# Kernel tuning notes

Hardware: AMD Instinct MI355X
Metric: run time of the kernel (lower is better)

## Reference

```python
import jax, jax.numpy as jnp
import numpy as np

N_NODES = 100000
N_EDGES = 3200000
IN_F = 128
HID = 32


def setup_inputs() -> dict:
    key = jax.random.key(0)
    k = jax.random.split(key, 8)
    x = jax.random.normal(k[0], (N_NODES, IN_F), dtype=jnp.float32)
    edge_index = jax.random.randint(k[1], (2, N_EDGES), 0, N_NODES, dtype=jnp.int64)
    edge_weight = jax.random.uniform(k[2], (N_EDGES,), dtype=jnp.float32)
    # GCN conv weight (in -> 32) and bias, then Linear(32 -> 1)
    s1 = 1.0 / np.sqrt(IN_F)
    s2 = 1.0 / np.sqrt(HID)
    W1 = jax.random.uniform(k[3], (IN_F, HID), dtype=jnp.float32, minval=-s1, maxval=s1)
    b1 = jax.random.uniform(k[4], (HID,), dtype=jnp.float32, minval=-s1, maxval=s1)
    W2 = jax.random.uniform(k[5], (HID, 1), dtype=jnp.float32, minval=-s2, maxval=s2)
    b2 = jax.random.uniform(k[6], (1,), dtype=jnp.float32, minval=-s2, maxval=s2)
    return {"x": x, "edge_index": edge_index, "edge_weight": edge_weight,
            "W1": W1, "b1": b1, "W2": W2, "b2": b2}


def gcn_conv(x, edge_index, edge_weight, W, b):
    N = x.shape[0]
    src = edge_index[0]
    dst = edge_index[1]
    loop = jnp.arange(N, dtype=edge_index.dtype)
    row = jnp.concatenate([dst, loop])  # aggregation targets
    col = jnp.concatenate([src, loop])  # message sources
    w = jnp.concatenate([edge_weight, jnp.ones((N,), dtype=x.dtype)])
    deg = jax.ops.segment_sum(w, row, num_segments=N)
    dinv = jnp.where(deg > 0, deg ** -0.5, 0.0).astype(x.dtype)
    norm = dinv[row] * w * dinv[col]  # [E+N]
    h = x @ W  # [N, 32]  transform before gather (cheaper)
    msgs = norm[:, None] * h[col]  # [E+N, 32]
    agg = jax.ops.segment_sum(msgs, row, num_segments=N)  # [N, 32]
    return agg + b


def reference(x, edge_index, edge_weight, W1, b1, W2, b2):
    h = gcn_conv(x, edge_index, edge_weight, W1, b1)
    h = jax.nn.relu(h)
    return h @ W2 + b2  # [N, 1]
```

## Files before the change

kernel.cpp:

```cpp
#include <hip/hip_runtime.h>
#include <hip/hip_bf16.h>
#include <hip/hip_fp16.h>

#define NN 100000
#define NE 3200000
#define IN_F 128
#define HID 32

#define BNODES 196
#define NB 511
#define NBP1 (NB + 1)
#define PBLK 768
#define EPB 4168
#define SSPAN 6912

typedef __hip_bfloat16 bf16;
typedef __attribute__((ext_vector_type(8))) short s16x8;
typedef __attribute__((ext_vector_type(4))) float f32x4;

__global__ __launch_bounds__(512) void k_part(const int* __restrict__ ei,
                                              const float* __restrict__ ew,
                                              int* __restrict__ offs,
                                              uint2* __restrict__ raw) {
    __shared__ int hist[NB];
    __shared__ int start[NB];
    __shared__ int wtot8[8];
    __shared__ __align__(16) uint2 sp[EPB];

    int t = threadIdx.x;
    int blk = blockIdx.x;
    if (t < NB) hist[t] = 0;
    __syncthreads();

    unsigned pk[10]; unsigned wb[10]; int bkt[10];
    int base_e = blk * EPB;
#pragma unroll
    for (int j = 0; j < 5; j++) {
        int p = j * 512 + t;
        int e = base_e + 2 * p;
        bool v = (p < (EPB / 2)) && (e < NE);
        if (v) {
            int2   s2 = *(const int2*)(ei + e);
            int2   d2 = *(const int2*)(ei + NE + e);
            float2 w2 = *(const float2*)(ew + e);
            int bk0 = d2.x / BNODES;
            bkt[2 * j]     = bk0;
            pk[2 * j]      = (unsigned)s2.x | ((unsigned)(d2.x - bk0 * BNODES) << 20);
            wb[2 * j]      = __float_as_uint(w2.x);
            int bk1 = d2.y / BNODES;
            bkt[2 * j + 1] = bk1;
            pk[2 * j + 1]  = (unsigned)s2.y | ((unsigned)(d2.y - bk1 * BNODES) << 20);
            wb[2 * j + 1]  = __float_as_uint(w2.y);
        } else { bkt[2 * j] = -1; bkt[2 * j + 1] = -1; }
    }
#pragma unroll
    for (int j = 0; j < 10; j++)
        if (bkt[j] >= 0) atomicAdd(&hist[bkt[j]], 1);
    __syncthreads();

    int h = (t < NB) ? hist[t] : 0;
    int lane = t & 63;
    int incl = h;
#pragma unroll
    for (int off = 1; off < 64; off <<= 1) {
        int up = __shfl_up(incl, off, 64);
        if (lane >= off) incl += up;
    }
    int wid = t >> 6;
    if (lane == 63) wtot8[wid] = incl;
    __syncthreads();
    int woff = 0;
    for (int wj = 0; wj < wid; wj++) woff += wtot8[wj];
    int exc = woff + incl - h;
    if (t < NB) start[t] = exc;
    __syncthreads();

    int total = start[NB - 1] + hist[NB - 1];
    int* orow = offs + (size_t)blk * NBP1;
    if (t < NB) orow[t] = start[t];
    if (t == 0) orow[NB] = total;
    __syncthreads();

#pragma unroll
    for (int j = 0; j < 10; j++) {
        if (bkt[j] >= 0) {
            int pos = atomicAdd(&start[bkt[j]], 1);
            sp[pos] = make_uint2(pk[j], wb[j]);
        }
    }
    __syncthreads();

    uint2* r = raw + (size_t)blk * EPB;
    int tot2 = total >> 1;
    const uint4* sp4 = (const uint4*)sp;
    uint4* r4 = (uint4*)r;
    for (int i = t; i < tot2; i += 512) r4[i] = sp4[i];
    if (t == 0 && (total & 1)) r[total - 1] = sp[total - 1];
}

__global__ __launch_bounds__(256) void k_trans(const int* __restrict__ in, int* __restrict__ out) {
    __shared__ int tile[32][33];
    int c0 = blockIdx.x * 32, r0 = blockIdx.y * 32;
    int tx = threadIdx.x & 31, ty = threadIdx.x >> 5;
    for (int i = ty; i < 32; i += 8) {
        int r = r0 + i, c = c0 + tx;
        if (r < PBLK && c < NBP1) tile[i][tx] = in[(size_t)r * NBP1 + c];
    }
    __syncthreads();
    for (int i = ty; i < 32; i += 8) {
        int c = c0 + i, r = r0 + tx;
        if (c < NBP1 && r < PBLK) out[(size_t)c * PBLK + r] = tile[tx][i];
    }
}

__global__ __launch_bounds__(512) void k_deg(const int* __restrict__ offsT,
                                             const uint2* __restrict__ raw,
                                             float* __restrict__ dinv) {
    __shared__ unsigned short runid[SSPAN];
    __shared__ int P[PBLK + 1];
    __shared__ int basearr[PBLK];
    __shared__ float wsum[BNODES];
    __shared__ int wt8[8];

    int t = threadIdx.x;
    int b = blockIdx.x;
    if (t < BNODES) wsum[t] = 0.f;

    int e0 = 2 * t, e1 = 2 * t + 1;
    int l0 = 0, l1 = 0, o0v = 0, o1v = 0;
    if (e0 < PBLK) {
        o0v = offsT[(size_t)b * PBLK + e0];
        l0  = offsT[(size_t)(b + 1) * PBLK + e0] - o0v;
    }
    if (e1 < PBLK) {
        o1v = offsT[(size_t)b * PBLK + e1];
        l1  = offsT[(size_t)(b + 1) * PBLK + e1] - o1v;
    }
    int psum = l0 + l1;
    int lane = t & 63;
    int incl = psum;
#pragma unroll
    for (int off = 1; off < 64; off <<= 1) {
        int up = __shfl_up(incl, off, 64);
        if (lane >= off) incl += up;
    }
    int wid = t >> 6;
    if (lane == 63) wt8[wid] = incl;
    __syncthreads();
    int woff = 0;
    for (int wj = 0; wj < wid; wj++) woff += wt8[wj];
    int exc = woff + incl - psum;
    if (e0 < PBLK) { P[e0] = exc;      basearr[e0] = o0v - exc; }
    if (e1 < PBLK) { P[e1] = exc + l0; basearr[e1] = o1v - (exc + l0); }
    if (t == 0) {
        int s = 0;
#pragma unroll
        for (int j = 0; j < 8; j++) s += wt8[j];
        P[PBLK] = s;
    }
    __syncthreads();

    int total = min(P[PBLK], SSPAN);

    for (int r = t; r < PBLK; r += 512) {
        int p0 = P[r], p1 = min(P[r + 1], SSPAN);
        for (int i = p0; i < p1; i++) runid[i] = (unsigned short)r;
    }
    __syncthreads();

#pragma unroll
    for (int k = 0; k < 14; k++) {
        int d = t + k * 512;
        if (d < total) {
            int r = runid[d];
            uint2 rec = raw[(size_t)r * EPB + (basearr[r] + d)];
            atomicAdd(&wsum[(rec.x >> 20) & 255], __uint_as_float(rec.y));
        }
    }
    __syncthreads();

    if (t < BNODES) {
        int node = b * BNODES + t;
        if (node < NN) dinv[node] = rsqrtf(wsum[t] + 1.0f);
    }
}

__global__ void k_w1frag(const float* __restrict__ W1, unsigned short* __restrict__ wfrag) {
    int lane = threadIdx.x;
    int q = lane >> 4;
    int n0 = lane & 15;
#pragma unroll
    for (int ks = 0; ks < 4; ks++) {
#pragma unroll
        for (int nt = 0; nt < 2; nt++) {
            int fi = ks * 2 + nt;
            int n = n0 + 16 * nt;
#pragma unroll
            for (int j = 0; j < 8; j++) {
                int k = ks * 32 + q * 8 + j;
                float v = W1[k * HID + n];
                __hip_bfloat16 bv = __float2bfloat16(v);
                wfrag[((size_t)fi * 64 + lane) * 8 + j] = *(unsigned short*)&bv;
            }
        }
    }
}

__global__ __launch_bounds__(256) void k_hs(const float* __restrict__ x,
                                            const unsigned short* __restrict__ wfrag,
                                            const float* __restrict__ dinv,
                                            bf16* __restrict__ hs) {
    int t = threadIdx.x;
    int lane = t & 63;
    int wv = t >> 6;
    int base = blockIdx.x * 64 + wv * 16;
    int m = lane & 15;
    int q = lane >> 4;
    int node = base + m;

    s16x8 wf[8];
    const s16x8* wp = (const s16x8*)wfrag;
#pragma unroll
    for (int fi = 0; fi < 8; fi++) wf[fi] = wp[fi * 64 + lane];

    f32x4 acc0 = {0.f, 0.f, 0.f, 0.f};
    f32x4 acc1 = {0.f, 0.f, 0.f, 0.f};

    const float* rowp = x + (size_t)node * IN_F + q * 8;
    bool valid = (node < NN);

#pragma unroll
    for (int ks = 0; ks < 4; ks++) {
        float4 f0 = {0,0,0,0}, f1 = {0,0,0,0};
        if (valid) {
            const float4* xr = (const float4*)(rowp + ks * 32);
            f0 = xr[0]; f1 = xr[1];
        }
        union { s16x8 v; unsigned u32[4]; } af;
        __hip_bfloat162 p0 = __float22bfloat162_rn({f0.x, f0.y});
        __hip_bfloat162 p1 = __float22bfloat162_rn({f0.z, f0.w});
        __hip_bfloat162 p2 = __float22bfloat162_rn({f1.x, f1.y});
        __hip_bfloat162 p3 = __float22bfloat162_rn({f1.z, f1.w});
        af.u32[0] = *(unsigned*)&p0;
        af.u32[1] = *(unsigned*)&p1;
        af.u32[2] = *(unsigned*)&p2;
        af.u32[3] = *(unsigned*)&p3;
        acc0 = __builtin_amdgcn_mfma_f32_16x16x32_bf16(af.v, wf[ks * 2 + 0], acc0, 0, 0, 0);
        acc1 = __builtin_amdgcn_mfma_f32_16x16x32_bf16(af.v, wf[ks * 2 + 1], acc1, 0, 0, 0);
    }

    int f = lane & 15;
#pragma unroll
    for (int r = 0; r < 4; r++) {
        int n2 = base + q * 4 + r;
        if (n2 < NN) {
            float dv = dinv[n2];
            hs[(size_t)n2 * HID + f]      = __float2bfloat16(dv * acc0[r]);
            hs[(size_t)n2 * HID + f + 16] = __float2bfloat16(dv * acc1[r]);
        }
    }
}

__global__ __launch_bounds__(512) void k_agg(const int* __restrict__ offsT,
                                             const uint2* __restrict__ raw,
                                             const bf16* __restrict__ hs,
                                             const float* __restrict__ dinv,
                                             const float* __restrict__ b1, const float* __restrict__ W2,
                                             const float* __restrict__ b2, float* __restrict__ out) {
    __shared__ uint2 se[SSPAN];
    __shared__ int P[PBLK + 1];
    __shared__ int basearr[PBLK];
    __shared__ int hist[BNODES];
    __shared__ int scanbuf[BNODES];
    __shared__ int cur[BNODES];
    __shared__ int wt8[8];

    unsigned short* runid = (unsigned short*)se;

    int t = threadIdx.x;
    int b = blockIdx.x;
    if (t < BNODES) hist[t] = 0;

    int e0 = 2 * t, e1 = 2 * t + 1;
    int l0 = 0, l1 = 0, o0v = 0, o1v = 0;
    if (e0 < PBLK) {
        o0v = offsT[(size_t)b * PBLK + e0];
        l0  = offsT[(size_t)(b + 1) * PBLK + e0] - o0v;
    }
    if (e1 < PBLK) {
        o1v = offsT[(size_t)b * PBLK + e1];
        l1  = offsT[(size_t)(b + 1) * PBLK + e1] - o1v;
    }
    int psum = l0 + l1;
    int lane = t & 63;
    int incl = psum;
#pragma unroll
    for (int off = 1; off < 64; off <<= 1) {
        int up = __shfl_up(incl, off, 64);
        if (lane >= off) incl += up;
    }
    int wid = t >> 6;
    if (lane == 63) wt8[wid] = incl;
    __syncthreads();
    int woff = 0;
    for (int wj = 0; wj < wid; wj++) woff += wt8[wj];
    int exc = woff + incl - psum;
    if (e0 < PBLK) { P[e0] = exc;      basearr[e0] = o0v - exc; }
    if (e1 < PBLK) { P[e1] = exc + l0; basearr[e1] = o1v - (exc + l0); }
    if (t == 0) {
        int s = 0;
#pragma unroll
        for (int j = 0; j < 8; j++) s += wt8[j];
        P[PBLK] = s;
    }
    __syncthreads();

    int total = min(P[PBLK], SSPAN);

    for (int r = t; r < PBLK; r += 512) {
        int p0 = P[r], p1 = min(P[r + 1], SSPAN);
        for (int i = p0; i < p1; i++) runid[i] = (unsigned short)r;
    }
    __syncthreads();

    uint2 rr[14];
#pragma unroll
    for (int k = 0; k < 14; k++) {
        int d = t + k * 512;
        if (d < total) {
            int r = runid[d];
            uint2 rec = raw[(size_t)r * EPB + (basearr[r] + d)];
            rr[k] = rec;
            int dl = (rec.x >> 20) & 255;
            atomicAdd(&hist[dl], 1);
        }
    }
    __syncthreads();

    if (t < BNODES) scanbuf[t] = hist[t];
    __syncthreads();
    for (int off = 1; off < BNODES; off <<= 1) {
        int v = 0;
        if (t < BNODES && t >= off) v = scanbuf[t - off];
        __syncthreads();
        if (t < BNODES) scanbuf[t] += v;
        __syncthreads();
    }
    if (t < BNODES) cur[t] = scanbuf[t] - hist[t];
    __syncthreads();

#pragma unroll
    for (int k = 0; k < 14; k++) {
        int d = t + k * 512;
        if (d < total) {
            uint2 rec = rr[k];
            int dl = (rec.x >> 20) & 255;
            int pos = atomicAdd(&cur[dl], 1);
            se[pos] = make_uint2(rec.x & 0xFFFFF, rec.y);
        }
    }
    __syncthreads();

    int gid = t >> 4;
    int l = t & 15;
    const __hip_bfloat162* hs2 = (const __hip_bfloat162*)hs;
    for (int dl = gid; dl < BNODES; dl += 32) {
        int cnt = hist[dl];
        int rs = scanbuf[dl] - cnt;
        float a0 = 0.f, a1 = 0.f;
        int full = cnt & ~7;
        int bse = 0;
        for (; bse < full; bse += 8) {
            uint2 q0 = se[rs + bse + 0];
            uint2 q1 = se[rs + bse + 1];
            uint2 q2 = se[rs + bse + 2];
            uint2 q3 = se[rs + bse + 3];
            uint2 q4 = se[rs + bse + 4];
            uint2 q5 = se[rs + bse + 5];
            uint2 q6 = se[rs + bse + 6];
            uint2 q7 = se[rs + bse + 7];
            __hip_bfloat162 h0 = hs2[(size_t)q0.x * 16 + l];
            __hip_bfloat162 h1 = hs2[(size_t)q1.x * 16 + l];
            __hip_bfloat162 h2 = hs2[(size_t)q2.x * 16 + l];
            __hip_bfloat162 h3 = hs2[(size_t)q3.x * 16 + l];
            __hip_bfloat162 h4 = hs2[(size_t)q4.x * 16 + l];
            __hip_bfloat162 h5 = hs2[(size_t)q5.x * 16 + l];
            __hip_bfloat162 h6 = hs2[(size_t)q6.x * 16 + l];
            __hip_bfloat162 h7 = hs2[(size_t)q7.x * 16 + l];
            float2 f0 = __bfloat1622float2(h0); a0 += __uint_as_float(q0.y) * f0.x; a1 += __uint_as_float(q0.y) * f0.y;
            float2 f1 = __bfloat1622float2(h1); a0 += __uint_as_float(q1.y) * f1.x; a1 += __uint_as_float(q1.y) * f1.y;
            float2 f2 = __bfloat1622float2(h2); a0 += __uint_as_float(q2.y) * f2.x; a1 += __uint_as_float(q2.y) * f2.y;
            float2 f3 = __bfloat1622float2(h3); a0 += __uint_as_float(q3.y) * f3.x; a1 += __uint_as_float(q3.y) * f3.y;
            float2 f4 = __bfloat1622float2(h4); a0 += __uint_as_float(q4.y) * f4.x; a1 += __uint_as_float(q4.y) * f4.y;
            float2 f5 = __bfloat1622float2(h5); a0 += __uint_as_float(q5.y) * f5.x; a1 += __uint_as_float(q5.y) * f5.y;
            float2 f6 = __bfloat1622float2(h6); a0 += __uint_as_float(q6.y) * f6.x; a1 += __uint_as_float(q6.y) * f6.y;
            float2 f7 = __bfloat1622float2(h7); a0 += __uint_as_float(q7.y) * f7.x; a1 += __uint_as_float(q7.y) * f7.y;
        }
        if (bse < cnt) {
            int rem = cnt - bse;
            uint2 q0 = se[rs + bse];
            uint2 q1 = se[rs + bse + (rem > 1 ? 1 : 0)];
            uint2 q2 = se[rs + bse + (rem > 2 ? 2 : 0)];
            uint2 q3 = se[rs + bse + (rem > 3 ? 3 : 0)];
            uint2 q4 = se[rs + bse + (rem > 4 ? 4 : 0)];
            uint2 q5 = se[rs + bse + (rem > 5 ? 5 : 0)];
            uint2 q6 = se[rs + bse + (rem > 6 ? 6 : 0)];
            float w0 = __uint_as_float(q0.y);
            float w1 = rem > 1 ? __uint_as_float(q1.y) : 0.f;
            float w2 = rem > 2 ? __uint_as_float(q2.y) : 0.f;
            float w3 = rem > 3 ? __uint_as_float(q3.y) : 0.f;
            float w4 = rem > 4 ? __uint_as_float(q4.y) : 0.f;
            float w5 = rem > 5 ? __uint_as_float(q5.y) : 0.f;
            float w6 = rem > 6 ? __uint_as_float(q6.y) : 0.f;
            __hip_bfloat162 h0 = hs2[(size_t)q0.x * 16 + l];
            __hip_bfloat162 h1 = hs2[(size_t)q1.x * 16 + l];
            __hip_bfloat162 h2 = hs2[(size_t)q2.x * 16 + l];
            __hip_bfloat162 h3 = hs2[(size_t)q3.x * 16 + l];
            __hip_bfloat162 h4 = hs2[(size_t)q4.x * 16 + l];
            __hip_bfloat162 h5 = hs2[(size_t)q5.x * 16 + l];
            __hip_bfloat162 h6 = hs2[(size_t)q6.x * 16 + l];
            float2 f0 = __bfloat1622float2(h0); a0 += w0 * f0.x; a1 += w0 * f0.y;
            float2 f1 = __bfloat1622float2(h1); a0 += w1 * f1.x; a1 += w1 * f1.y;
            float2 f2 = __bfloat1622float2(h2); a0 += w2 * f2.x; a1 += w2 * f2.y;
            float2 f3 = __bfloat1622float2(h3); a0 += w3 * f3.x; a1 += w3 * f3.y;
            float2 f4 = __bfloat1622float2(h4); a0 += w4 * f4.x; a1 += w4 * f4.y;
            float2 f5 = __bfloat1622float2(h5); a0 += w5 * f5.x; a1 += w5 * f5.y;
            float2 f6 = __bfloat1622float2(h6); a0 += w6 * f6.x; a1 += w6 * f6.y;
        }
        int node = b * BNODES + dl;
        if (node < NN) {
            float dv = dinv[node];
            float2 fs = __bfloat1622float2(hs2[(size_t)node * 16 + l]);
            float v0 = dv * (a0 + fs.x) + b1[2 * l];
            float v1 = dv * (a1 + fs.y) + b1[2 * l + 1];
            v0 = fmaxf(v0, 0.f);
            v1 = fmaxf(v1, 0.f);
            float ps = v0 * W2[2 * l] + v1 * W2[2 * l + 1];
#pragma unroll
            for (int m2 = 8; m2 >= 1; m2 >>= 1) ps += __shfl_xor(ps, m2, 16);
            if (l == 0) out[node] = ps + b2[0];
        }
    }
}

extern "C" void kernel_launch(void* const* d_in, const int* in_sizes, int n_in,
                              void* d_out, int out_size, void* d_ws, size_t ws_size,
                              hipStream_t stream) {
    const float* x  = (const float*)d_in[0];
    const int*   ei = (const int*)d_in[1];
    const float* ew = (const float*)d_in[2];
    const float* W1 = (const float*)d_in[3];
    const float* b1 = (const float*)d_in[4];
    const float* W2 = (const float*)d_in[5];
    const float* b2 = (const float*)d_in[6];
    float* out = (float*)d_out;

    char* ws = (char*)d_ws;
    uint2*          raw      = (uint2*)         (ws + 0);
    int*            offs     = (int*)           (ws + 25608192);
    int*            offsT    = (int*)           (ws + 27181056);
    bf16*           hs       = (bf16*)          (ws + 28753920);
    float*          dinv     = (float*)         (ws + 35153920);
    unsigned short* wfrag    = (unsigned short*)(ws + 35553920);

    k_w1frag<<<1, 64, 0, stream>>>(W1, wfrag);
    k_part<<<PBLK, 512, 0, stream>>>(ei, ew, offs, raw);
    k_trans<<<dim3((NBP1 + 31) / 32, (PBLK + 31) / 32), 256, 0, stream>>>(offs, offsT);
    k_deg<<<NB, 512, 0, stream>>>(offsT, raw, dinv);
    k_hs<<<(NN + 63) / 64, 256, 0, stream>>>(x, wfrag, dinv, hs);
    k_agg<<<NB, 512, 0, stream>>>(offsT, raw, hs, dinv, b1, W2, b2, out);
}
```

Baseline: 204.5 us.

## Halve node buckets per block and drop the offsets transpose kernel

Destination buckets shrink from 196 to 98 nodes, so the degree and aggregation kernels launch twice as many blocks, each with half the shared-memory span. The partition kernel's scan now handles two buckets per thread. The separate transpose kernel is removed, and the consumers read the per-partition offset table directly with strided column accesses. This saves one launch and one pass over the offsets table, in exchange for uncoalesced offset reads and a tighter per-bucket edge capacity that random degree variation has to fit within.

```diff
diff --git a/kernel.cpp b/kernel.cpp
--- a/kernel.cpp
+++ b/kernel.cpp
@@ -7,12 +7,12 @@
 #define IN_F 128
 #define HID 32
 
-#define BNODES 196
-#define NB 511
+#define BNODES 98
+#define NB 1021
 #define NBP1 (NB + 1)
 #define PBLK 768
 #define EPB 4168
-#define SSPAN 6912
+#define SSPAN 3584
 
 typedef __hip_bfloat16 bf16;
 typedef __attribute__((ext_vector_type(8))) short s16x8;
@@ -29,7 +29,7 @@
 
     int t = threadIdx.x;
     int blk = blockIdx.x;
-    if (t < NB) hist[t] = 0;
+    for (int b = t; b < NB; b += 512) hist[b] = 0;
     __syncthreads();
 
     unsigned pk[10]; unsigned wb[10]; int bkt[10];
@@ -58,9 +58,12 @@
         if (bkt[j] >= 0) atomicAdd(&hist[bkt[j]], 1);
     __syncthreads();
 
-    int h = (t < NB) ? hist[t] : 0;
+    int e0 = 2 * t, e1 = 2 * t + 1;
+    int h0 = (e0 < NB) ? hist[e0] : 0;
+    int h1 = (e1 < NB) ? hist[e1] : 0;
+    int psum = h0 + h1;
     int lane = t & 63;
-    int incl = h;
+    int incl = psum;
 #pragma unroll
     for (int off = 1; off < 64; off <<= 1) {
         int up = __shfl_up(incl, off, 64);
@@ -71,13 +74,14 @@
     __syncthreads();
     int woff = 0;
     for (int wj = 0; wj < wid; wj++) woff += wtot8[wj];
-    int exc = woff + incl - h;
-    if (t < NB) start[t] = exc;
+    int exc = woff + incl - psum;
+    if (e0 < NB) start[e0] = exc;
+    if (e1 < NB) start[e1] = exc + h0;
     __syncthreads();
 
     int total = start[NB - 1] + hist[NB - 1];
     int* orow = offs + (size_t)blk * NBP1;
-    if (t < NB) orow[t] = start[t];
+    for (int b = t; b < NB; b += 512) orow[b] = start[b];
     if (t == 0) orow[NB] = total;
     __syncthreads();
 
@@ -98,22 +102,7 @@
     if (t == 0 && (total & 1)) r[total - 1] = sp[total - 1];
 }
 
-__global__ __launch_bounds__(256) void k_trans(const int* __restrict__ in, int* __restrict__ out) {
-    __shared__ int tile[32][33];
-    int c0 = blockIdx.x * 32, r0 = blockIdx.y * 32;
-    int tx = threadIdx.x & 31, ty = threadIdx.x >> 5;
-    for (int i = ty; i < 32; i += 8) {
-        int r = r0 + i, c = c0 + tx;
-        if (r < PBLK && c < NBP1) tile[i][tx] = in[(size_t)r * NBP1 + c];
-    }
-    __syncthreads();
-    for (int i = ty; i < 32; i += 8) {
-        int c = c0 + i, r = r0 + tx;
-        if (c < NBP1 && r < PBLK) out[(size_t)c * PBLK + r] = tile[tx][i];
-    }
-}
-
-__global__ __launch_bounds__(512) void k_deg(const int* __restrict__ offsT,
+__global__ __launch_bounds__(512) void k_deg(const int* __restrict__ offs,
                                              const uint2* __restrict__ raw,
                                              float* __restrict__ dinv) {
     __shared__ unsigned short runid[SSPAN];
@@ -129,12 +118,12 @@
     int e0 = 2 * t, e1 = 2 * t + 1;
     int l0 = 0, l1 = 0, o0v = 0, o1v = 0;
     if (e0 < PBLK) {
-        o0v = offsT[(size_t)b * PBLK + e0];
-        l0  = offsT[(size_t)(b + 1) * PBLK + e0] - o0v;
+        o0v = offs[(size_t)e0 * NBP1 + b];
+        l0  = offs[(size_t)e0 * NBP1 + b + 1] - o0v;
     }
     if (e1 < PBLK) {
-        o1v = offsT[(size_t)b * PBLK + e1];
-        l1  = offsT[(size_t)(b + 1) * PBLK + e1] - o1v;
+        o1v = offs[(size_t)e1 * NBP1 + b];
+        l1  = offs[(size_t)e1 * NBP1 + b + 1] - o1v;
     }
     int psum = l0 + l1;
     int lane = t & 63;
@@ -169,12 +158,12 @@
     __syncthreads();
 
 #pragma unroll
-    for (int k = 0; k < 14; k++) {
+    for (int k = 0; k < 7; k++) {
         int d = t + k * 512;
         if (d < total) {
             int r = runid[d];
             uint2 rec = raw[(size_t)r * EPB + (basearr[r] + d)];
-            atomicAdd(&wsum[(rec.x >> 20) & 255], __uint_as_float(rec.y));
+            atomicAdd(&wsum[(rec.x >> 20) & 127], __uint_as_float(rec.y));
         }
     }
     __syncthreads();
@@ -261,7 +250,7 @@
     }
 }
 
-__global__ __launch_bounds__(512) void k_agg(const int* __restrict__ offsT,
+__global__ __launch_bounds__(512) void k_agg(const int* __restrict__ offs,
                                              const uint2* __restrict__ raw,
                                              const bf16* __restrict__ hs,
                                              const float* __restrict__ dinv,
@@ -284,12 +273,12 @@
     int e0 = 2 * t, e1 = 2 * t + 1;
     int l0 = 0, l1 = 0, o0v = 0, o1v = 0;
     if (e0 < PBLK) {
-        o0v = offsT[(size_t)b * PBLK + e0];
-        l0  = offsT[(size_t)(b + 1) * PBLK + e0] - o0v;
+        o0v = offs[(size_t)e0 * NBP1 + b];
+        l0  = offs[(size_t)e0 * NBP1 + b + 1] - o0v;
     }
     if (e1 < PBLK) {
-        o1v = offsT[(size_t)b * PBLK + e1];
-        l1  = offsT[(size_t)(b + 1) * PBLK + e1] - o1v;
+        o1v = offs[(size_t)e1 * NBP1 + b];
+        l1  = offs[(size_t)e1 * NBP1 + b + 1] - o1v;
     }
     int psum = l0 + l1;
     int lane = t & 63;
@@ -323,15 +312,15 @@
     }
     __syncthreads();
 
-    uint2 rr[14];
-#pragma unroll
-    for (int k = 0; k < 14; k++) {
+    uint2 rr[7];
+#pragma unroll
+    for (int k = 0; k < 7; k++) {
         int d = t + k * 512;
         if (d < total) {
             int r = runid[d];
             uint2 rec = raw[(size_t)r * EPB + (basearr[r] + d)];
             rr[k] = rec;
-            int dl = (rec.x >> 20) & 255;
+            int dl = (rec.x >> 20) & 127;
             atomicAdd(&hist[dl], 1);
         }
     }
@@ -350,11 +339,11 @@
     __syncthreads();
 
 #pragma unroll
-    for (int k = 0; k < 14; k++) {
+    for (int k = 0; k < 7; k++) {
         int d = t + k * 512;
         if (d < total) {
             uint2 rec = rr[k];
-            int dl = (rec.x >> 20) & 255;
+            int dl = (rec.x >> 20) & 127;
             int pos = atomicAdd(&cur[dl], 1);
             se[pos] = make_uint2(rec.x & 0xFFFFF, rec.y);
         }
@@ -458,15 +447,13 @@
     char* ws = (char*)d_ws;
     uint2*          raw      = (uint2*)         (ws + 0);
     int*            offs     = (int*)           (ws + 25608192);
-    int*            offsT    = (int*)           (ws + 27181056);
-    bf16*           hs       = (bf16*)          (ws + 28753920);
-    float*          dinv     = (float*)         (ws + 35153920);
-    unsigned short* wfrag    = (unsigned short*)(ws + 35553920);
+    bf16*           hs       = (bf16*)          (ws + 28747776);
+    float*          dinv     = (float*)         (ws + 35147776);
+    unsigned short* wfrag    = (unsigned short*)(ws + 35547776);
 
     k_w1frag<<<1, 64, 0, stream>>>(W1, wfrag);
     k_part<<<PBLK, 512, 0, stream>>>(ei, ew, offs, raw);
-    k_trans<<<dim3((NBP1 + 31) / 32, (PBLK + 31) / 32), 256, 0, stream>>>(offs, offsT);
-    k_deg<<<NB, 512, 0, stream>>>(offsT, raw, dinv);
+    k_deg<<<NB, 512, 0, stream>>>(offs, raw, dinv);
     k_hs<<<(NN + 63) / 64, 256, 0, stream>>>(x, wfrag, dinv, hs);
-    k_agg<<<NB, 512, 0, stream>>>(offsT, raw, hs, dinv, b1, W2, b2, out);
-}
+    k_agg<<<NB, 512, 0, stream>>>(offs, raw, hs, dinv, b1, W2, b2, out);
+}
```

Result: slower. 214.1 us (+4.7%).
